# Performance work log

Hardware: AMD Instinct MI355X
Metric: run time of the kernel (lower is better)

The kernel has to match this reference:

```python
import jax, jax.numpy as jnp
import numpy as np
import math

B, N, HIDDEN = 2, 2048, 896
H_Q, H_KV, D = 14, 2, 64
ROPE_BASE = 1000000.0


def setup_inputs() -> dict:
    key = jax.random.key(0)
    ks = jax.random.split(key, 6)
    s = 0.02  # typical init scale for transformer weights
    return {
        "hidden_states": jax.random.normal(ks[0], (B, N, HIDDEN), jnp.float32),
        "position_ids": jnp.broadcast_to(jnp.arange(N, dtype=jnp.int32), (B, N)),
        "q_w": jax.random.normal(ks[1], (HIDDEN, H_Q * D), jnp.float32) * s,
        "q_b": jnp.zeros((H_Q * D,), jnp.float32),
        "k_w": jax.random.normal(ks[2], (HIDDEN, H_KV * D), jnp.float32) * s,
        "k_b": jnp.zeros((H_KV * D,), jnp.float32),
        "v_w": jax.random.normal(ks[3], (HIDDEN, H_KV * D), jnp.float32) * s,
        "v_b": jnp.zeros((H_KV * D,), jnp.float32),
        "o_w": jax.random.normal(ks[4], (H_Q * D, HIDDEN), jnp.float32) * s,
    }


def _rope(x, cos, sin):
    # rotate_half: [x1, x2] -> [-x2, x1]
    x1, x2 = jnp.split(x, 2, axis=-1)
    return x * cos + jnp.concatenate([-x2, x1], axis=-1) * sin


def reference(hidden_states, position_ids, q_w, q_b, k_w, k_b, v_w, v_b, o_w):
    Bs, Ns, _ = hidden_states.shape
    g = H_Q // H_KV  # heads per KV group (GQA)
    # QKV projections -> [B, H, N, d]
    Q = (hidden_states @ q_w + q_b).reshape(Bs, Ns, H_Q, D).transpose(0, 2, 1, 3)
    K = (hidden_states @ k_w + k_b).reshape(Bs, Ns, H_KV, D).transpose(0, 2, 1, 3)
    V = (hidden_states @ v_w + v_b).reshape(Bs, Ns, H_KV, D).transpose(0, 2, 1, 3)
    # RoPE (NTK base=1e6), cached cos/sin gathered by position_ids
    inv_freq = 1.0 / (ROPE_BASE ** (jnp.arange(0, D, 2, dtype=jnp.float32) / D))
    freqs = position_ids.astype(jnp.float32)[..., None] * inv_freq  # [B, N, D/2]
    emb = jnp.concatenate([freqs, freqs], axis=-1)  # [B, N, D]
    cos = jnp.cos(emb)[:, None]  # [B, 1, N, D]
    sin = jnp.sin(emb)[:, None]
    Q = _rope(Q, cos, sin)
    K = _rope(K, cos, sin)
    # GQA attention without materializing expanded K/V: group Q by KV head
    Qg = Q.reshape(Bs, H_KV, g, Ns, D)
    scale = 1.0 / math.sqrt(D)
    S = jnp.einsum('bkgqd,bknd->bkgqn', Qg, K) * scale  # [B, Hkv, g, Nq, Nk]
    # kv_cache=None => q_global_start = 0 => standard causal mask
    causal = jnp.arange(Ns)[:, None] >= jnp.arange(Ns)[None, :]
    S = jnp.where(causal[None, None, None], S, -jnp.inf)
    # stable softmax matching the module's online-softmax result (l + 1e-8)
    m = jnp.max(S, axis=-1, keepdims=True)
    e = jnp.exp(S - m)
    l = jnp.sum(e, axis=-1, keepdims=True)
    O = jnp.einsum('bkgqn,bknd->bkgqd', e, V) / (l + 1e-8)
    O = O.reshape(Bs, H_Q, Ns, D).transpose(0, 2, 1, 3).reshape(Bs, Ns, H_Q * D)
    return O @ o_w  # [B, N, hidden]
```

## Files before the change

kernel.cpp:

```cpp
#include <hip/hip_runtime.h>
#include <math.h>

#define BB 2
#define NN 2048
#define HID 896
#define HQ 14
#define HKV 2
#define DD 64
#define QKV_COLS 1152
#define QSCALE 0.18033688011112042f

typedef __bf16 bf16x8 __attribute__((ext_vector_type(8)));
typedef float f32x4 __attribute__((ext_vector_type(4)));

__device__ inline ushort f2bs(float f) {
  uint u = __builtin_bit_cast(uint, f);
  u += 0x7FFFu + ((u >> 16) & 1u);
  return (ushort)(u >> 16);
}
__device__ inline float bs2f(ushort u) {
  return __builtin_bit_cast(float, (uint)u << 16);
}

__device__ inline void gload16(const ushort* g, ushort* l) {
  __builtin_amdgcn_global_load_lds(
      (const __attribute__((address_space(1))) uint*)g,
      (__attribute__((address_space(3))) uint*)l, 16, 0, 0);
}

__device__ inline float dpp_fmax16(float x) {
  int v;
  v = __builtin_amdgcn_update_dpp(0, __builtin_bit_cast(int, x), 0xB1, 0xF, 0xF, true);
  x = fmaxf(x, __builtin_bit_cast(float, v));
  v = __builtin_amdgcn_update_dpp(0, __builtin_bit_cast(int, x), 0x4E, 0xF, 0xF, true);
  x = fmaxf(x, __builtin_bit_cast(float, v));
  v = __builtin_amdgcn_update_dpp(0, __builtin_bit_cast(int, x), 0x124, 0xF, 0xF, true);
  x = fmaxf(x, __builtin_bit_cast(float, v));
  v = __builtin_amdgcn_update_dpp(0, __builtin_bit_cast(int, x), 0x128, 0xF, 0xF, true);
  x = fmaxf(x, __builtin_bit_cast(float, v));
  return x;
}
__device__ inline float dpp_fadd16(float x) {
  int v;
  v = __builtin_amdgcn_update_dpp(0, __builtin_bit_cast(int, x), 0xB1, 0xF, 0xF, true);
  x += __builtin_bit_cast(float, v);
  v = __builtin_amdgcn_update_dpp(0, __builtin_bit_cast(int, x), 0x4E, 0xF, 0xF, true);
  x += __builtin_bit_cast(float, v);
  v = __builtin_amdgcn_update_dpp(0, __builtin_bit_cast(int, x), 0x124, 0xF, 0xF, true);
  x += __builtin_bit_cast(float, v);
  v = __builtin_amdgcn_update_dpp(0, __builtin_bit_cast(int, x), 0x128, 0xF, 0xF, true);
  x += __builtin_bit_cast(float, v);
  return x;
}

__global__ __launch_bounds__(256)
void prep_kernel(const float* __restrict__ hid, const int* __restrict__ pos,
                 const float* __restrict__ qw, const float* __restrict__ kw,
                 const float* __restrict__ vw, const float* __restrict__ ow,
                 const float* __restrict__ qb, const float* __restrict__ kb,
                 const float* __restrict__ vb,
                 ushort* __restrict__ Ah, ushort* __restrict__ WqkvT,
                 ushort* __restrict__ WoT, float2* __restrict__ tab,
                 float* __restrict__ biasQ)
{
  __shared__ float tile[32][33];
  const int blk = blockIdx.x, t = threadIdx.x;
  if (blk < 3584) {
    int i = blk * 256 + t;
    float4 v = ((const float4*)hid)[i];
    ushort4 o;
    o.x = f2bs(v.x); o.y = f2bs(v.y); o.z = f2bs(v.z); o.w = f2bs(v.w);
    ((ushort4*)Ah)[i] = o;
  } else if (blk < 5376) {
    const float* src; int N, n0, drow, k0;
    if (blk < 4592) {
      int idx = blk - 3584;
      int bx = idx % 36; k0 = (idx / 36) * 32;
      if (bx < 28)      { src = qw; N = 896; n0 = bx * 32;        drow = n0; }
      else if (bx < 32) { src = kw; N = 128; n0 = (bx - 28) * 32; drow = 896 + n0; }
      else              { src = vw; N = 128; n0 = (bx - 32) * 32; drow = 1024 + n0; }
    } else {
      int idx = blk - 4592;
      src = ow; N = 896; n0 = (idx % 28) * 32; k0 = (idx / 28) * 32; drow = n0;
    }
    ushort* dst = (blk < 4592) ? WqkvT : WoT;
    const int tx = t & 31, ty = t >> 5;
#pragma unroll
    for (int i = 0; i < 32; i += 8)
      tile[ty + i][tx] = src[(size_t)(k0 + ty + i) * N + n0 + tx];
    __syncthreads();
#pragma unroll
    for (int i = 0; i < 32; i += 8)
      dst[(size_t)(drow + ty + i) * HID + k0 + tx] = f2bs(tile[tx][ty + i]);
  } else if (blk < 5888) {
    int idx = (blk - 5376) * 256 + t;
    int m = idx >> 5, f = idx & 31;
    float inv = exp2f(-(float)f * (19.9315685693241741f / 32.0f));
    float ang = (float)pos[m] * inv;
    float sv, cv;
    sincosf(ang, &sv, &cv);
    tab[idx] = make_float2(cv, sv);
  } else {
    int i = (blk - 5888) * 256 + t;
    if (i < QKV_COLS)
      biasQ[i] = (i < 896) ? qb[i] : (i < 1024 ? kb[i - 896] : vb[i - 1024]);
  }
}

__global__ __launch_bounds__(256)
void gemm_qkv_rope(const ushort* __restrict__ A, const ushort* __restrict__ Bt,
                   const float* __restrict__ biasQ, const float2* __restrict__ tab,
                   ushort* __restrict__ Qo, ushort* __restrict__ Ko,
                   ushort* __restrict__ Vto)
{
  __shared__ ushort smem[9216];
  ushort* As = smem;
  ushort* Bs = smem + 2048;
  const int bx = blockIdx.x;
  const int n0 = bx * 128;
  const int m0 = blockIdx.y * 64;
  const int t = threadIdx.x;
  const int w = t >> 6, lane = t & 63;
  const int quad = lane >> 4, nn = lane & 15;
  const int wm = (w & 1) * 32, wn = (w >> 1) * 64;

  f32x4 acc[2][4];
#pragma unroll
  for (int i = 0; i < 2; i++)
#pragma unroll
    for (int j = 0; j < 4; j++) acc[i][j] = (f32x4){0.f, 0.f, 0.f, 0.f};

  for (int k0 = 0; k0 < HID; k0 += 32) {
    __syncthreads();
#pragma unroll
    for (int c = 0; c < 3; c++) {
      int ch = w * 3 + c;
      int rr = (lane >> 2), cl = lane & 3;
      if (ch < 4) {
        int r = ch * 16 + rr;
        int cg = cl ^ ((r >> 1) & 3);
        gload16(A + (size_t)(m0 + r) * HID + k0 + cg * 8, &As[r * 32 + cl * 8]);
      } else {
        int r = (ch - 4) * 16 + rr;
        int cg = cl ^ ((r >> 1) & 3);
        gload16(Bt + (size_t)(n0 + r) * HID + k0 + cg * 8, &Bs[r * 32 + cl * 8]);
      }
    }
    __syncthreads();

    bf16x8 aF[2], bF[4];
#pragma unroll
    for (int i = 0; i < 2; i++) {
      int ra = wm + i * 16 + nn;
      aF[i] = *(const bf16x8*)(&As[ra * 32 + (quad ^ ((ra >> 1) & 3)) * 8]);
    }
#pragma unroll
    for (int j = 0; j < 4; j++) {
      int rb = wn + j * 16 + nn;
      bF[j] = *(const bf16x8*)(&Bs[rb * 32 + (quad ^ ((rb >> 1) & 3)) * 8]);
    }
#pragma unroll
    for (int i = 0; i < 2; i++)
#pragma unroll
      for (int j = 0; j < 4; j++)
        acc[i][j] = __builtin_amdgcn_mfma_f32_16x16x32_bf16(aF[i], bF[j], acc[i][j], 0, 0, 0);
  }

  float bv[4];
#pragma unroll
  for (int j = 0; j < 4; j++) bv[j] = biasQ[n0 + wn + j * 16 + nn];

  if (bx < 8) {
    const float qs = (bx < 7) ? QSCALE : 1.0f;
    __syncthreads();
    const int ht = w >> 1;
    ushort* T = smem + ht * 4224;
#pragma unroll
    for (int i = 0; i < 2; i++) {
#pragma unroll
      for (int r = 0; r < 4; r++) {
        int row = wm + i * 16 + quad * 4 + r;
        int m = m0 + row;
        float2 cs0 = tab[m * 32 + nn];
        float2 cs1 = tab[m * 32 + 16 + nn];
        float x0 = (acc[i][0][r] + bv[0]) * qs;
        float x1 = (acc[i][1][r] + bv[1]) * qs;
        float x2 = (acc[i][2][r] + bv[2]) * qs;
        float x3 = (acc[i][3][r] + bv[3]) * qs;
        T[row * 66 + nn]      = f2bs(x0 * cs0.x - x2 * cs0.y);
        T[row * 66 + 16 + nn] = f2bs(x1 * cs1.x - x3 * cs1.y);
        T[row * 66 + 32 + nn] = f2bs(x2 * cs0.x + x0 * cs0.y);
        T[row * 66 + 48 + nn] = f2bs(x3 * cs1.x + x1 * cs1.y);
      }
    }
    __syncthreads();
    const int ht2 = t >> 7, tl = t & 127, row2 = tl >> 1, col0 = (tl & 1) * 32;
    const int m = m0 + row2, b = m >> 11, n = m & (NN - 1);
    const int hg = bx * 2 + ht2;
    ushort* dst = (hg < HQ)
        ? Qo + ((size_t)(b * HQ + hg) * NN + n) * DD + col0
        : Ko + ((size_t)(b * HKV + (hg - HQ)) * NN + n) * DD + col0;
    const ushort* src = smem + ht2 * 4224 + row2 * 66 + col0;
#pragma unroll
    for (int u = 0; u < 4; u++) ((uint4*)dst)[u] = ((const uint4*)src)[u];
  } else {
    __syncthreads();
    const int kvh = wn >> 6;
    ushort* T = smem + kvh * (64 * 72);
#pragma unroll
    for (int j = 0; j < 4; j++) {
      int dd = j * 16 + nn;
      float bvj = bv[j];
#pragma unroll
      for (int i = 0; i < 2; i++) {
        int mloc = wm + i * 16 + quad * 4;
        ushort4 pk;
        pk.x = f2bs(acc[i][j][0] + bvj);
        pk.y = f2bs(acc[i][j][1] + bvj);
        pk.z = f2bs(acc[i][j][2] + bvj);
        pk.w = f2bs(acc[i][j][3] + bvj);
        *(ushort4*)(&T[dd * 72 + mloc]) = pk;
      }
    }
    __syncthreads();
    const int head = t >> 7, dd2 = (t >> 1) & 63, seg = t & 1;
    const int b = m0 >> 11, nbase = (m0 & (NN - 1)) + seg * 32;
    const ushort* src = smem + head * (64 * 72) + dd2 * 72 + seg * 32;
    ushort* d = Vto + ((size_t)(b * HKV + head) * DD + dd2) * NN + nbase;
#pragma unroll
    for (int u = 0; u < 4; u++) ((uint4*)d)[u] = ((const uint4*)src)[u];
  }
}

__global__ __launch_bounds__(256)
void gemm_o(const ushort* __restrict__ A, const ushort* __restrict__ Bt,
            float* __restrict__ out)
{
  const int n0 = blockIdx.x * 128;
  const int m0 = blockIdx.y * 64;
  __shared__ ushort As[64 * 32];
  __shared__ ushort Bs[128 * 32];
  const int t = threadIdx.x;
  const int w = t >> 6, lane = t & 63;
  const int quad = lane >> 4, nn = lane & 15;
  const int wm = (w & 1) * 32, wn = (w >> 1) * 64;

  f32x4 acc[2][4];
#pragma unroll
  for (int i = 0; i < 2; i++)
#pragma unroll
    for (int j = 0; j < 4; j++) acc[i][j] = (f32x4){0.f, 0.f, 0.f, 0.f};

  for (int k0 = 0; k0 < HID; k0 += 32) {
    __syncthreads();
#pragma unroll
    for (int c = 0; c < 3; c++) {
      int ch = w * 3 + c;
      int rr = (lane >> 2), cl = lane & 3;
      if (ch < 4) {
        int r = ch * 16 + rr;
        int cg = cl ^ ((r >> 1) & 3);
        gload16(A + (size_t)(m0 + r) * HID + k0 + cg * 8, &As[r * 32 + cl * 8]);
      } else {
        int r = (ch - 4) * 16 + rr;
        int cg = cl ^ ((r >> 1) & 3);
        gload16(Bt + (size_t)(n0 + r) * HID + k0 + cg * 8, &Bs[r * 32 + cl * 8]);
      }
    }
    __syncthreads();

    bf16x8 aF[2], bF[4];
#pragma unroll
    for (int i = 0; i < 2; i++) {
      int ra = wm + i * 16 + nn;
      aF[i] = *(const bf16x8*)(&As[ra * 32 + (quad ^ ((ra >> 1) & 3)) * 8]);
    }
#pragma unroll
    for (int j = 0; j < 4; j++) {
      int rb = wn + j * 16 + nn;
      bF[j] = *(const bf16x8*)(&Bs[rb * 32 + (quad ^ ((rb >> 1) & 3)) * 8]);
    }
#pragma unroll
    for (int i = 0; i < 2; i++)
#pragma unroll
      for (int j = 0; j < 4; j++)
        acc[i][j] = __builtin_amdgcn_mfma_f32_16x16x32_bf16(aF[i], bF[j], acc[i][j], 0, 0, 0);
  }

#pragma unroll
  for (int j = 0; j < 4; j++) {
    const int col = n0 + wn + j * 16 + nn;
#pragma unroll
    for (int i = 0; i < 2; i++) {
      const int row = m0 + wm + i * 16 + quad * 4;
#pragma unroll
      for (int r = 0; r < 4; r++)
        out[(size_t)(row + r) * HID + col] = acc[i][j][r];
    }
  }
}

template <bool DIAG>
__device__ __forceinline__ void attn_step(
    int j, int qt, int quad, int nn,
    const ushort* __restrict__ Kb, const ushort* __restrict__ Vtb,
    ushort* __restrict__ Ps, const bf16x8 (&aQ)[2][2],
    f32x4 (&acc)[2][4], float (&mst)[2][4], float (&lac)[2][4])
{
  bf16x8 bk0[4], bk1[4];
#pragma unroll
  for (int ct = 0; ct < 4; ct++) {
    const ushort* kr = Kb + (size_t)(j * 64 + ct * 16 + nn) * DD;
    bk0[ct] = *(const bf16x8*)(kr + quad * 8);
    bk1[ct] = *(const bf16x8*)(kr + 32 + quad * 8);
  }
  bf16x8 bv0[4], bv1[4];
#pragma unroll
  for (int dt = 0; dt < 4; dt++) {
    const ushort* vr = Vtb + (size_t)(dt * 16 + nn) * NN + j * 64;
    bv0[dt] = *(const bf16x8*)(vr + quad * 8);
    bv1[dt] = *(const bf16x8*)(vr + 32 + quad * 8);
  }

  f32x4 s[2][4];
#pragma unroll
  for (int ct = 0; ct < 4; ct++)
#pragma unroll
    for (int mt = 0; mt < 2; mt++) {
      f32x4 cc = __builtin_amdgcn_mfma_f32_16x16x32_bf16(
          aQ[mt][0], bk0[ct], (f32x4){0.f, 0.f, 0.f, 0.f}, 0, 0, 0);
      s[mt][ct] = __builtin_amdgcn_mfma_f32_16x16x32_bf16(aQ[mt][1], bk1[ct], cc, 0, 0, 0);
    }

  if (DIAG) {
    const int keyb = j * 64 + nn;
    const int qb_ = qt * 32 + quad * 4;
#pragma unroll
    for (int mt = 0; mt < 2; mt++)
#pragma unroll
      for (int ct = 0; ct < 4; ct++)
#pragma unroll
        for (int r = 0; r < 4; r++)
          if (keyb + ct * 16 > qb_ + mt * 16 + r) s[mt][ct][r] = -1e30f;
  }

#pragma unroll
  for (int mt = 0; mt < 2; mt++)
#pragma unroll
    for (int r = 0; r < 4; r++) {
      float mx = fmaxf(fmaxf(s[mt][0][r], s[mt][1][r]), fmaxf(s[mt][2][r], s[mt][3][r]));
      mx = dpp_fmax16(mx);
      float mn = fmaxf(mst[mt][r], mx);
      float alpha = exp2f(mst[mt][r] - mn);
      mst[mt][r] = mn;
      float ll = 0.f;
#pragma unroll
      for (int ct = 0; ct < 4; ct++) {
        float p = exp2f(s[mt][ct][r] - mn);
        s[mt][ct][r] = p;
        ll += p;
      }
      lac[mt][r] = lac[mt][r] * alpha + ll;
#pragma unroll
      for (int dt = 0; dt < 4; dt++) acc[mt][dt][r] *= alpha;
    }

#pragma unroll
  for (int mt = 0; mt < 2; mt++)
#pragma unroll
    for (int ct = 0; ct < 4; ct++)
#pragma unroll
      for (int r = 0; r < 4; r++)
        Ps[(mt * 16 + quad * 4 + r) * 66 + ct * 16 + nn] = f2bs(s[mt][ct][r]);

#pragma unroll
  for (int mt = 0; mt < 2; mt++) {
    bf16x8 aP0 = *(const bf16x8*)(&Ps[(mt * 16 + nn) * 66 + quad * 8]);
    bf16x8 aP1 = *(const bf16x8*)(&Ps[(mt * 16 + nn) * 66 + 32 + quad * 8]);
#pragma unroll
    for (int dt = 0; dt < 4; dt++) {
      acc[mt][dt] = __builtin_amdgcn_mfma_f32_16x16x32_bf16(aP0, bv0[dt], acc[mt][dt], 0, 0, 0);
      acc[mt][dt] = __builtin_amdgcn_mfma_f32_16x16x32_bf16(aP1, bv1[dt], acc[mt][dt], 0, 0, 0);
    }
  }
}

__global__ __launch_bounds__(64, 3)
void attn_kernel(const ushort* __restrict__ Q, const ushort* __restrict__ K,
                 const ushort* __restrict__ Vt, ushort* __restrict__ O,
                 ushort* __restrict__ Opart, float* __restrict__ mpart,
                 float* __restrict__ lpart)
{
  const int u = 107 - (int)blockIdx.x;
  int qt, c;
  if (u < 28)      { qt = u; c = 0; }
  else if (u < 84) { int v = u - 28; qt = 28 + (v >> 1); c = v & 1; }
  else             { int v = u - 84; qt = 56 + v / 3; c = v - (v / 3) * 3; }
  const int h = blockIdx.y, b = blockIdx.z;
  const int kvh = h / (HQ / HKV);
  const int q0 = qt * 32;
  const int jmax = qt >> 1;
  const int nc = jmax / 14 + 1;
  const int jlo = c * 14;
  const int jhi = min(jmax, jlo + 13);
  const bool hasdiag = (jhi == jmax);
  const int jB = hasdiag ? jmax : jhi + 1;

  __shared__ ushort Ps[32 * 66];

  const int lane = threadIdx.x;
  const int quad = lane >> 4, nn = lane & 15;

  const ushort* Qb = Q + ((size_t)(b * HQ + h) * NN + q0) * DD;
  bf16x8 aQ[2][2];
#pragma unroll
  for (int mt = 0; mt < 2; mt++)
#pragma unroll
    for (int ks = 0; ks < 2; ks++)
      aQ[mt][ks] = *(const bf16x8*)(Qb + (size_t)(mt * 16 + nn) * DD + ks * 32 + quad * 8);

  const ushort* Kb  = K  + (size_t)(b * HKV + kvh) * NN * DD;
  const ushort* Vtb = Vt + (size_t)(b * HKV + kvh) * DD * NN;

  f32x4 acc[2][4];
#pragma unroll
  for (int mt = 0; mt < 2; mt++)
#pragma unroll
    for (int dt = 0; dt < 4; dt++) acc[mt][dt] = (f32x4){0.f, 0.f, 0.f, 0.f};
  float mst[2][4], lac[2][4];
#pragma unroll
  for (int mt = 0; mt < 2; mt++)
#pragma unroll
    for (int r = 0; r < 4; r++) { mst[mt][r] = -1e30f; lac[mt][r] = 0.f; }

  for (int j = jlo; j < jB; j++)
    attn_step<false>(j, qt, quad, nn, Kb, Vtb, Ps, aQ, acc, mst, lac);
  if (hasdiag)
    attn_step<true>(jmax, qt, quad, nn, Kb, Vtb, Ps, aQ, acc, mst, lac);

  float ltot[2][4];
#pragma unroll
  for (int mt = 0; mt < 2; mt++)
#pragma unroll
    for (int r = 0; r < 4; r++) ltot[mt][r] = dpp_fadd16(lac[mt][r]);

  if (nc == 1) {
#pragma unroll
    for (int mt = 0; mt < 2; mt++)
#pragma unroll
      for (int r = 0; r < 4; r++) {
        float linv = 1.f / (ltot[mt][r] + 1e-8f);
#pragma unroll
        for (int dt = 0; dt < 4; dt++)
          O[(size_t)(b * NN + q0 + mt * 16 + quad * 4 + r) * HID + h * DD + dt * 16 + nn] =
              f2bs(acc[mt][dt][r] * linv);
      }
  } else {
    const int off = (qt < 56) ? (qt - 28) * 2 : 56 + (qt - 56) * 3;
    const int p = (b * HQ + h) * 80 + off + c;
    ushort* Op = Opart + (size_t)p * 2048;
#pragma unroll
    for (int mt = 0; mt < 2; mt++)
#pragma unroll
      for (int r = 0; r < 4; r++) {
#pragma unroll
        for (int dt = 0; dt < 4; dt++)
          Op[(mt * 16 + quad * 4 + r) * 64 + dt * 16 + nn] = f2bs(acc[mt][dt][r]);
        if (nn == 0) {
          mpart[(size_t)p * 32 + mt * 16 + quad * 4 + r] = mst[mt][r];
          lpart[(size_t)p * 32 + mt * 16 + quad * 4 + r] = ltot[mt][r];
        }
      }
  }
}

__global__ __launch_bounds__(256)
void attn_reduce_kernel(const ushort* __restrict__ Opart, const float* __restrict__ mpart,
                        const float* __restrict__ lpart, ushort* __restrict__ O)
{
  const int qt = 28 + blockIdx.x;
  const int h = blockIdx.y, b = blockIdx.z;
  const int nc = (qt < 56) ? 2 : 3;
  const int off = (qt < 56) ? (qt - 28) * 2 : 56 + (qt - 56) * 3;
  const int pb = (b * HQ + h) * 80 + off;
  const int t = threadIdx.x;
  const int row = t >> 3, seg = t & 7;

  float mv[3], lv[3];
  float M = -1e30f;
  for (int c = 0; c < nc; c++) {
    mv[c] = mpart[(size_t)(pb + c) * 32 + row];
    lv[c] = lpart[(size_t)(pb + c) * 32 + row];
    M = fmaxf(M, mv[c]);
  }
  float l = 0.f, wv[3];
  for (int c = 0; c < nc; c++) { wv[c] = exp2f(mv[c] - M); l += lv[c] * wv[c]; }
  const float linv = 1.f / (l + 1e-8f);

  float av[8];
#pragma unroll
  for (int k = 0; k < 8; k++) av[k] = 0.f;
  for (int c = 0; c < nc; c++) {
    const ushort* Op = Opart + (size_t)(pb + c) * 2048 + row * 64 + seg * 8;
#pragma unroll
    for (int k = 0; k < 8; k++) av[k] += wv[c] * bs2f(Op[k]);
  }
  ushort ov[8];
#pragma unroll
  for (int k = 0; k < 8; k++) ov[k] = f2bs(av[k] * linv);
  ushort* Od = O + (size_t)(b * NN + qt * 32 + row) * HID + h * DD + seg * 8;
  *(uint4*)Od = *(uint4*)ov;
}

extern "C" void kernel_launch(void* const* d_in, const int* in_sizes, int n_in,
                              void* d_out, int out_size, void* d_ws, size_t ws_size,
                              hipStream_t stream)
{
  const float* hid = (const float*)d_in[0];
  const int*   pos = (const int*)  d_in[1];
  const float* qw  = (const float*)d_in[2];
  const float* qb  = (const float*)d_in[3];
  const float* kw  = (const float*)d_in[4];
  const float* kb  = (const float*)d_in[5];
  const float* vw  = (const float*)d_in[6];
  const float* vb  = (const float*)d_in[7];
  const float* ow  = (const float*)d_in[8];
  float* outp = (float*)d_out;

  ushort* WoT   = (ushort*)d_ws;
  ushort* WqkvT = WoT   + (size_t)HID * HID;
  ushort* Ah    = WqkvT + (size_t)QKV_COLS * HID;
  ushort* Qb    = Ah    + (size_t)4096 * HID;
  ushort* Kb    = Qb    + (size_t)BB * HQ  * NN * DD;
  ushort* Vtb   = Kb    + (size_t)BB * HKV * NN * DD;
  ushort* Ob    = Vtb   + (size_t)BB * HKV * NN * DD;
  float2* tab   = (float2*)(Ob + (size_t)4096 * HID);
  float*  biasQ = (float*)(tab + (size_t)4096 * 32);
  float*  mpart = biasQ + QKV_COLS;
  float*  lpart = mpart + (size_t)2240 * 32;
  ushort* Opart = WqkvT;

  prep_kernel<<<dim3(5893), 256, 0, stream>>>(hid, pos, qw, kw, vw, ow, qb, kb, vb,
                                              Ah, WqkvT, WoT, tab, biasQ);
  gemm_qkv_rope<<<dim3(9, 64), 256, 0, stream>>>(Ah, WqkvT, biasQ, tab, Qb, Kb, Vtb);
  attn_kernel<<<dim3(108, HQ, BB), 64, 0, stream>>>(Qb, Kb, Vtb, Ob, Opart, mpart, lpart);
  attn_reduce_kernel<<<dim3(36, HQ, BB), 256, 0, stream>>>(Opart, mpart, lpart, Ob);
  gemm_o<<<dim3(HID / 128, 64), 256, 0, stream>>>(Ob, WoT, outp);
}
```

Measured before the change: 215.7 us.

## Shrink attention query tile to 16 rows, add lazy rescale and MFMA priority

The attention kernel now processes 16 query rows per wave instead of 32. This doubles the grid to 216 blocks per head and raises the occupancy hint to 5 waves, with the split-K partition and reduce kernel remapped to match. It also skips the online-softmax rescale unless some row's max grows by more than 8, and raises wave priority around the MFMA sections. The cost is that each K/V tile loaded from global memory is reused across half as many queries, which doubles K/V traffic.

New measurement: 326.6 us. 51.4% more time.

```diff
diff --git a/kernel.cpp b/kernel.cpp
--- a/kernel.cpp
+++ b/kernel.cpp
@@ -301,11 +301,11 @@
 }
 
 template <bool DIAG>
-__device__ __forceinline__ void attn_step(
-    int j, int qt, int quad, int nn,
+__device__ __forceinline__ void attn_step16(
+    int j, int qglob, int quad, int nn,
     const ushort* __restrict__ Kb, const ushort* __restrict__ Vtb,
-    ushort* __restrict__ Ps, const bf16x8 (&aQ)[2][2],
-    f32x4 (&acc)[2][4], float (&mst)[2][4], float (&lac)[2][4])
+    ushort* __restrict__ Ps, const bf16x8 (&aQ)[2],
+    f32x4 (&acc)[4], float (&mst)[4], float (&lac)[4])
 {
   bf16x8 bk0[4], bk1[4];
 #pragma unroll
@@ -322,175 +322,169 @@
     bv1[dt] = *(const bf16x8*)(vr + 32 + quad * 8);
   }
 
-  f32x4 s[2][4];
-#pragma unroll
-  for (int ct = 0; ct < 4; ct++)
-#pragma unroll
-    for (int mt = 0; mt < 2; mt++) {
-      f32x4 cc = __builtin_amdgcn_mfma_f32_16x16x32_bf16(
-          aQ[mt][0], bk0[ct], (f32x4){0.f, 0.f, 0.f, 0.f}, 0, 0, 0);
-      s[mt][ct] = __builtin_amdgcn_mfma_f32_16x16x32_bf16(aQ[mt][1], bk1[ct], cc, 0, 0, 0);
-    }
+  f32x4 s[4];
+  __builtin_amdgcn_s_setprio(1);
+#pragma unroll
+  for (int ct = 0; ct < 4; ct++) {
+    f32x4 cc = __builtin_amdgcn_mfma_f32_16x16x32_bf16(
+        aQ[0], bk0[ct], (f32x4){0.f, 0.f, 0.f, 0.f}, 0, 0, 0);
+    s[ct] = __builtin_amdgcn_mfma_f32_16x16x32_bf16(aQ[1], bk1[ct], cc, 0, 0, 0);
+  }
+  __builtin_amdgcn_s_setprio(0);
 
   if (DIAG) {
     const int keyb = j * 64 + nn;
-    const int qb_ = qt * 32 + quad * 4;
-#pragma unroll
-    for (int mt = 0; mt < 2; mt++)
-#pragma unroll
-      for (int ct = 0; ct < 4; ct++)
-#pragma unroll
-        for (int r = 0; r < 4; r++)
-          if (keyb + ct * 16 > qb_ + mt * 16 + r) s[mt][ct][r] = -1e30f;
-  }
-
-#pragma unroll
-  for (int mt = 0; mt < 2; mt++)
+#pragma unroll
+    for (int ct = 0; ct < 4; ct++)
+#pragma unroll
+      for (int r = 0; r < 4; r++)
+        if (keyb + ct * 16 > qglob + r) s[ct][r] = -1e30f;
+  }
+
+  float mx[4];
+#pragma unroll
+  for (int r = 0; r < 4; r++)
+    mx[r] = dpp_fmax16(fmaxf(fmaxf(fmaxf(s[0][r], s[1][r]), s[2][r]), s[3][r]));
+
+  bool grow = false;
+#pragma unroll
+  for (int r = 0; r < 4; r++) grow = grow || (mx[r] > mst[r] + 8.0f);
+  if (__any(grow)) {
 #pragma unroll
     for (int r = 0; r < 4; r++) {
-      float mx = fmaxf(fmaxf(s[mt][0][r], s[mt][1][r]), fmaxf(s[mt][2][r], s[mt][3][r]));
-      mx = dpp_fmax16(mx);
-      float mn = fmaxf(mst[mt][r], mx);
-      float alpha = exp2f(mst[mt][r] - mn);
-      mst[mt][r] = mn;
-      float ll = 0.f;
-#pragma unroll
-      for (int ct = 0; ct < 4; ct++) {
-        float p = exp2f(s[mt][ct][r] - mn);
-        s[mt][ct][r] = p;
-        ll += p;
-      }
-      lac[mt][r] = lac[mt][r] * alpha + ll;
-#pragma unroll
-      for (int dt = 0; dt < 4; dt++) acc[mt][dt][r] *= alpha;
-    }
-
-#pragma unroll
-  for (int mt = 0; mt < 2; mt++)
-#pragma unroll
-    for (int ct = 0; ct < 4; ct++)
-#pragma unroll
-      for (int r = 0; r < 4; r++)
-        Ps[(mt * 16 + quad * 4 + r) * 66 + ct * 16 + nn] = f2bs(s[mt][ct][r]);
-
-#pragma unroll
-  for (int mt = 0; mt < 2; mt++) {
-    bf16x8 aP0 = *(const bf16x8*)(&Ps[(mt * 16 + nn) * 66 + quad * 8]);
-    bf16x8 aP1 = *(const bf16x8*)(&Ps[(mt * 16 + nn) * 66 + 32 + quad * 8]);
-#pragma unroll
-    for (int dt = 0; dt < 4; dt++) {
-      acc[mt][dt] = __builtin_amdgcn_mfma_f32_16x16x32_bf16(aP0, bv0[dt], acc[mt][dt], 0, 0, 0);
-      acc[mt][dt] = __builtin_amdgcn_mfma_f32_16x16x32_bf16(aP1, bv1[dt], acc[mt][dt], 0, 0, 0);
-    }
-  }
-}
-
-__global__ __launch_bounds__(64, 3)
+      float mn = fmaxf(mst[r], mx[r]);
+      float alpha = exp2f(mst[r] - mn);
+      mst[r] = mn;
+      lac[r] *= alpha;
+#pragma unroll
+      for (int dt = 0; dt < 4; dt++) acc[dt][r] *= alpha;
+    }
+  }
+
+#pragma unroll
+  for (int r = 0; r < 4; r++) {
+    float ll = 0.f;
+#pragma unroll
+    for (int ct = 0; ct < 4; ct++) {
+      float p = exp2f(s[ct][r] - mst[r]);
+      s[ct][r] = p;
+      ll += p;
+    }
+    lac[r] += ll;
+  }
+
+#pragma unroll
+  for (int ct = 0; ct < 4; ct++)
+#pragma unroll
+    for (int r = 0; r < 4; r++)
+      Ps[(quad * 4 + r) * 66 + ct * 16 + nn] = f2bs(s[ct][r]);
+
+  bf16x8 aP0 = *(const bf16x8*)(&Ps[nn * 66 + quad * 8]);
+  bf16x8 aP1 = *(const bf16x8*)(&Ps[nn * 66 + 32 + quad * 8]);
+  __builtin_amdgcn_s_setprio(1);
+#pragma unroll
+  for (int dt = 0; dt < 4; dt++) {
+    acc[dt] = __builtin_amdgcn_mfma_f32_16x16x32_bf16(aP0, bv0[dt], acc[dt], 0, 0, 0);
+    acc[dt] = __builtin_amdgcn_mfma_f32_16x16x32_bf16(aP1, bv1[dt], acc[dt], 0, 0, 0);
+  }
+  __builtin_amdgcn_s_setprio(0);
+}
+
+__global__ __launch_bounds__(64, 5)
 void attn_kernel(const ushort* __restrict__ Q, const ushort* __restrict__ K,
                  const ushort* __restrict__ Vt, ushort* __restrict__ O,
                  ushort* __restrict__ Opart, float* __restrict__ mpart,
                  float* __restrict__ lpart)
 {
-  const int u = 107 - (int)blockIdx.x;
+  const int u = 215 - (int)blockIdx.x;
   int qt, c;
-  if (u < 28)      { qt = u; c = 0; }
-  else if (u < 84) { int v = u - 28; qt = 28 + (v >> 1); c = v & 1; }
-  else             { int v = u - 84; qt = 56 + v / 3; c = v - (v / 3) * 3; }
+  if (u < 56)       { qt = u; c = 0; }
+  else if (u < 168) { int v = u - 56; qt = 56 + (v >> 1); c = v & 1; }
+  else              { int v = u - 168; qt = 112 + v / 3; c = v - (v / 3) * 3; }
   const int h = blockIdx.y, b = blockIdx.z;
   const int kvh = h / (HQ / HKV);
-  const int q0 = qt * 32;
-  const int jmax = qt >> 1;
+  const int q0 = qt * 16;
+  const int jmax = qt >> 2;
   const int nc = jmax / 14 + 1;
   const int jlo = c * 14;
   const int jhi = min(jmax, jlo + 13);
   const bool hasdiag = (jhi == jmax);
   const int jB = hasdiag ? jmax : jhi + 1;
 
-  __shared__ ushort Ps[32 * 66];
+  __shared__ ushort Ps[16 * 66];
 
   const int lane = threadIdx.x;
   const int quad = lane >> 4, nn = lane & 15;
+  const int qglob = q0 + quad * 4;
 
   const ushort* Qb = Q + ((size_t)(b * HQ + h) * NN + q0) * DD;
-  bf16x8 aQ[2][2];
-#pragma unroll
-  for (int mt = 0; mt < 2; mt++)
-#pragma unroll
-    for (int ks = 0; ks < 2; ks++)
-      aQ[mt][ks] = *(const bf16x8*)(Qb + (size_t)(mt * 16 + nn) * DD + ks * 32 + quad * 8);
+  bf16x8 aQ[2];
+#pragma unroll
+  for (int ks = 0; ks < 2; ks++)
+    aQ[ks] = *(const bf16x8*)(Qb + (size_t)nn * DD + ks * 32 + quad * 8);
 
   const ushort* Kb  = K  + (size_t)(b * HKV + kvh) * NN * DD;
   const ushort* Vtb = Vt + (size_t)(b * HKV + kvh) * DD * NN;
 
-  f32x4 acc[2][4];
-#pragma unroll
-  for (int mt = 0; mt < 2; mt++)
-#pragma unroll
-    for (int dt = 0; dt < 4; dt++) acc[mt][dt] = (f32x4){0.f, 0.f, 0.f, 0.f};
-  float mst[2][4], lac[2][4];
-#pragma unroll
-  for (int mt = 0; mt < 2; mt++)
-#pragma unroll
-    for (int r = 0; r < 4; r++) { mst[mt][r] = -1e30f; lac[mt][r] = 0.f; }
+  f32x4 acc[4];
+#pragma unroll
+  for (int dt = 0; dt < 4; dt++) acc[dt] = (f32x4){0.f, 0.f, 0.f, 0.f};
+  float mst[4], lac[4];
+#pragma unroll
+  for (int r = 0; r < 4; r++) { mst[r] = -1e30f; lac[r] = 0.f; }
 
   for (int j = jlo; j < jB; j++)
-    attn_step<false>(j, qt, quad, nn, Kb, Vtb, Ps, aQ, acc, mst, lac);
+    attn_step16<false>(j, qglob, quad, nn, Kb, Vtb, Ps, aQ, acc, mst, lac);
   if (hasdiag)
-    attn_step<true>(jmax, qt, quad, nn, Kb, Vtb, Ps, aQ, acc, mst, lac);
-
-  float ltot[2][4];
-#pragma unroll
-  for (int mt = 0; mt < 2; mt++)
-#pragma unroll
-    for (int r = 0; r < 4; r++) ltot[mt][r] = dpp_fadd16(lac[mt][r]);
+    attn_step16<true>(jmax, qglob, quad, nn, Kb, Vtb, Ps, aQ, acc, mst, lac);
+
+  float ltot[4];
+#pragma unroll
+  for (int r = 0; r < 4; r++) ltot[r] = dpp_fadd16(lac[r]);
 
   if (nc == 1) {
 #pragma unroll
-    for (int mt = 0; mt < 2; mt++)
-#pragma unroll
-      for (int r = 0; r < 4; r++) {
-        float linv = 1.f / (ltot[mt][r] + 1e-8f);
-#pragma unroll
-        for (int dt = 0; dt < 4; dt++)
-          O[(size_t)(b * NN + q0 + mt * 16 + quad * 4 + r) * HID + h * DD + dt * 16 + nn] =
-              f2bs(acc[mt][dt][r] * linv);
+    for (int r = 0; r < 4; r++) {
+      float linv = 1.f / (ltot[r] + 1e-8f);
+#pragma unroll
+      for (int dt = 0; dt < 4; dt++)
+        O[(size_t)(b * NN + q0 + quad * 4 + r) * HID + h * DD + dt * 16 + nn] =
+            f2bs(acc[dt][r] * linv);
+    }
+  } else {
+    const int off = (qt < 112) ? (qt - 56) * 2 : 112 + (qt - 112) * 3;
+    const int p = (b * HQ + h) * 160 + off + c;
+    ushort* Op = Opart + (size_t)p * 1024;
+#pragma unroll
+    for (int r = 0; r < 4; r++) {
+#pragma unroll
+      for (int dt = 0; dt < 4; dt++)
+        Op[(quad * 4 + r) * 64 + dt * 16 + nn] = f2bs(acc[dt][r]);
+      if (nn == 0) {
+        mpart[(size_t)p * 16 + quad * 4 + r] = mst[r];
+        lpart[(size_t)p * 16 + quad * 4 + r] = ltot[r];
       }
-  } else {
-    const int off = (qt < 56) ? (qt - 28) * 2 : 56 + (qt - 56) * 3;
-    const int p = (b * HQ + h) * 80 + off + c;
-    ushort* Op = Opart + (size_t)p * 2048;
-#pragma unroll
-    for (int mt = 0; mt < 2; mt++)
-#pragma unroll
-      for (int r = 0; r < 4; r++) {
-#pragma unroll
-        for (int dt = 0; dt < 4; dt++)
-          Op[(mt * 16 + quad * 4 + r) * 64 + dt * 16 + nn] = f2bs(acc[mt][dt][r]);
-        if (nn == 0) {
-          mpart[(size_t)p * 32 + mt * 16 + quad * 4 + r] = mst[mt][r];
-          lpart[(size_t)p * 32 + mt * 16 + quad * 4 + r] = ltot[mt][r];
-        }
-      }
-  }
-}
-
-__global__ __launch_bounds__(256)
+    }
+  }
+}
+
+__global__ __launch_bounds__(128)
 void attn_reduce_kernel(const ushort* __restrict__ Opart, const float* __restrict__ mpart,
                         const float* __restrict__ lpart, ushort* __restrict__ O)
 {
-  const int qt = 28 + blockIdx.x;
+  const int qt = 56 + blockIdx.x;
   const int h = blockIdx.y, b = blockIdx.z;
-  const int nc = (qt < 56) ? 2 : 3;
-  const int off = (qt < 56) ? (qt - 28) * 2 : 56 + (qt - 56) * 3;
-  const int pb = (b * HQ + h) * 80 + off;
+  const int nc = (qt < 112) ? 2 : 3;
+  const int off = (qt < 112) ? (qt - 56) * 2 : 112 + (qt - 112) * 3;
+  const int pb = (b * HQ + h) * 160 + off;
   const int t = threadIdx.x;
   const int row = t >> 3, seg = t & 7;
 
   float mv[3], lv[3];
   float M = -1e30f;
   for (int c = 0; c < nc; c++) {
-    mv[c] = mpart[(size_t)(pb + c) * 32 + row];
-    lv[c] = lpart[(size_t)(pb + c) * 32 + row];
+    mv[c] = mpart[(size_t)(pb + c) * 16 + row];
+    lv[c] = lpart[(size_t)(pb + c) * 16 + row];
     M = fmaxf(M, mv[c]);
   }
   float l = 0.f, wv[3];
@@ -501,14 +495,14 @@
 #pragma unroll
   for (int k = 0; k < 8; k++) av[k] = 0.f;
   for (int c = 0; c < nc; c++) {
-    const ushort* Op = Opart + (size_t)(pb + c) * 2048 + row * 64 + seg * 8;
+    const ushort* Op = Opart + (size_t)(pb + c) * 1024 + row * 64 + seg * 8;
 #pragma unroll
     for (int k = 0; k < 8; k++) av[k] += wv[c] * bs2f(Op[k]);
   }
   ushort ov[8];
 #pragma unroll
   for (int k = 0; k < 8; k++) ov[k] = f2bs(av[k] * linv);
-  ushort* Od = O + (size_t)(b * NN + qt * 32 + row) * HID + h * DD + seg * 8;
+  ushort* Od = O + (size_t)(b * NN + qt * 16 + row) * HID + h * DD + seg * 8;
   *(uint4*)Od = *(uint4*)ov;
 }
 
@@ -537,13 +531,13 @@
   float2* tab   = (float2*)(Ob + (size_t)4096 * HID);
   float*  biasQ = (float*)(tab + (size_t)4096 * 32);
   float*  mpart = biasQ + QKV_COLS;
-  float*  lpart = mpart + (size_t)2240 * 32;
+  float*  lpart = mpart + (size_t)4480 * 16;
   ushort* Opart = WqkvT;
 
   prep_kernel<<<dim3(5893), 256, 0, stream>>>(hid, pos, qw, kw, vw, ow, qb, kb, vb,
                                               Ah, WqkvT, WoT, tab, biasQ);
   gemm_qkv_rope<<<dim3(9, 64), 256, 0, stream>>>(Ah, WqkvT, biasQ, tab, Qb, Kb, Vtb);
-  attn_kernel<<<dim3(108, HQ, BB), 64, 0, stream>>>(Qb, Kb, Vtb, Ob, Opart, mpart, lpart);
-  attn_reduce_kernel<<<dim3(36, HQ, BB), 256, 0, stream>>>(Opart, mpart, lpart, Ob);
+  attn_kernel<<<dim3(216, HQ, BB), 64, 0, stream>>>(Qb, Kb, Vtb, Ob, Opart, mpart, lpart);
+  attn_reduce_kernel<<<dim3(72, HQ, BB), 128, 0, stream>>>(Opart, mpart, lpart, Ob);
   gemm_o<<<dim3(HID / 128, 64), 256, 0, stream>>>(Ob, WoT, outp);
 }
```

## Prefetch next K tile in registers, lazy softmax rescale, MFMA priority hints

Applied to the files above, without the earlier changes.

Loads the next iteration's K fragments during the current attention step, so global-load latency overlaps with compute. Online-softmax rescaling of the accumulators is skipped unless some row max grows by more than 8 in log2 units; the stale max is used otherwise. s_setprio is raised around the MFMA blocks. The prefetch raises register pressure and issues one extra K load at the end of each block. The lazy rescale relies on the bounded growth of exponent values staying within fp32 range.

Result: slower. 264.4 us (+22.6%).

```diff
diff --git a/kernel.cpp b/kernel.cpp
--- a/kernel.cpp
+++ b/kernel.cpp
@@ -302,18 +302,12 @@
 
 template <bool DIAG>
 __device__ __forceinline__ void attn_step(
-    int j, int qt, int quad, int nn,
+    int j, int jn, int qt, int quad, int nn,
     const ushort* __restrict__ Kb, const ushort* __restrict__ Vtb,
     ushort* __restrict__ Ps, const bf16x8 (&aQ)[2][2],
+    bf16x8 (&bk0)[4], bf16x8 (&bk1)[4],
     f32x4 (&acc)[2][4], float (&mst)[2][4], float (&lac)[2][4])
 {
-  bf16x8 bk0[4], bk1[4];
-#pragma unroll
-  for (int ct = 0; ct < 4; ct++) {
-    const ushort* kr = Kb + (size_t)(j * 64 + ct * 16 + nn) * DD;
-    bk0[ct] = *(const bf16x8*)(kr + quad * 8);
-    bk1[ct] = *(const bf16x8*)(kr + 32 + quad * 8);
-  }
   bf16x8 bv0[4], bv1[4];
 #pragma unroll
   for (int dt = 0; dt < 4; dt++) {
@@ -321,8 +315,16 @@
     bv0[dt] = *(const bf16x8*)(vr + quad * 8);
     bv1[dt] = *(const bf16x8*)(vr + 32 + quad * 8);
   }
+  bf16x8 nk0[4], nk1[4];
+#pragma unroll
+  for (int ct = 0; ct < 4; ct++) {
+    const ushort* kr = Kb + (size_t)(jn * 64 + ct * 16 + nn) * DD;
+    nk0[ct] = *(const bf16x8*)(kr + quad * 8);
+    nk1[ct] = *(const bf16x8*)(kr + 32 + quad * 8);
+  }
 
   f32x4 s[2][4];
+  __builtin_amdgcn_s_setprio(1);
 #pragma unroll
   for (int ct = 0; ct < 4; ct++)
 #pragma unroll
@@ -331,6 +333,7 @@
           aQ[mt][0], bk0[ct], (f32x4){0.f, 0.f, 0.f, 0.f}, 0, 0, 0);
       s[mt][ct] = __builtin_amdgcn_mfma_f32_16x16x32_bf16(aQ[mt][1], bk1[ct], cc, 0, 0, 0);
     }
+  __builtin_amdgcn_s_setprio(0);
 
   if (DIAG) {
     const int keyb = j * 64 + nn;
@@ -344,25 +347,45 @@
           if (keyb + ct * 16 > qb_ + mt * 16 + r) s[mt][ct][r] = -1e30f;
   }
 
+  float mx[2][4];
+#pragma unroll
+  for (int mt = 0; mt < 2; mt++)
+#pragma unroll
+    for (int r = 0; r < 4; r++)
+      mx[mt][r] = dpp_fmax16(
+          fmaxf(fmaxf(s[mt][0][r], s[mt][1][r]), fmaxf(s[mt][2][r], s[mt][3][r])));
+
+  bool grow = false;
+#pragma unroll
+  for (int mt = 0; mt < 2; mt++)
+#pragma unroll
+    for (int r = 0; r < 4; r++) grow = grow || (mx[mt][r] > mst[mt][r] + 8.0f);
+  if (__any(grow)) {
+#pragma unroll
+    for (int mt = 0; mt < 2; mt++)
+#pragma unroll
+      for (int r = 0; r < 4; r++) {
+        float mn = fmaxf(mst[mt][r], mx[mt][r]);
+        float alpha = exp2f(mst[mt][r] - mn);
+        mst[mt][r] = mn;
+        lac[mt][r] *= alpha;
+#pragma unroll
+        for (int dt = 0; dt < 4; dt++) acc[mt][dt][r] *= alpha;
+      }
+  }
+
 #pragma unroll
   for (int mt = 0; mt < 2; mt++)
 #pragma unroll
     for (int r = 0; r < 4; r++) {
-      float mx = fmaxf(fmaxf(s[mt][0][r], s[mt][1][r]), fmaxf(s[mt][2][r], s[mt][3][r]));
-      mx = dpp_fmax16(mx);
-      float mn = fmaxf(mst[mt][r], mx);
-      float alpha = exp2f(mst[mt][r] - mn);
-      mst[mt][r] = mn;
       float ll = 0.f;
 #pragma unroll
       for (int ct = 0; ct < 4; ct++) {
-        float p = exp2f(s[mt][ct][r] - mn);
+        float p = exp2f(s[mt][ct][r] - mst[mt][r]);
         s[mt][ct][r] = p;
         ll += p;
       }
-      lac[mt][r] = lac[mt][r] * alpha + ll;
-#pragma unroll
-      for (int dt = 0; dt < 4; dt++) acc[mt][dt][r] *= alpha;
+      lac[mt][r] += ll;
     }
 
 #pragma unroll
@@ -377,12 +400,17 @@
   for (int mt = 0; mt < 2; mt++) {
     bf16x8 aP0 = *(const bf16x8*)(&Ps[(mt * 16 + nn) * 66 + quad * 8]);
     bf16x8 aP1 = *(const bf16x8*)(&Ps[(mt * 16 + nn) * 66 + 32 + quad * 8]);
+    __builtin_amdgcn_s_setprio(1);
 #pragma unroll
     for (int dt = 0; dt < 4; dt++) {
       acc[mt][dt] = __builtin_amdgcn_mfma_f32_16x16x32_bf16(aP0, bv0[dt], acc[mt][dt], 0, 0, 0);
       acc[mt][dt] = __builtin_amdgcn_mfma_f32_16x16x32_bf16(aP1, bv1[dt], acc[mt][dt], 0, 0, 0);
     }
-  }
+    __builtin_amdgcn_s_setprio(0);
+  }
+
+#pragma unroll
+  for (int ct = 0; ct < 4; ct++) { bk0[ct] = nk0[ct]; bk1[ct] = nk1[ct]; }
 }
 
 __global__ __launch_bounds__(64, 3)
@@ -433,10 +461,18 @@
 #pragma unroll
     for (int r = 0; r < 4; r++) { mst[mt][r] = -1e30f; lac[mt][r] = 0.f; }
 
+  bf16x8 bk0[4], bk1[4];
+#pragma unroll
+  for (int ct = 0; ct < 4; ct++) {
+    const ushort* kr = Kb + (size_t)(jlo * 64 + ct * 16 + nn) * DD;
+    bk0[ct] = *(const bf16x8*)(kr + quad * 8);
+    bk1[ct] = *(const bf16x8*)(kr + 32 + quad * 8);
+  }
+
   for (int j = jlo; j < jB; j++)
-    attn_step<false>(j, qt, quad, nn, Kb, Vtb, Ps, aQ, acc, mst, lac);
+    attn_step<false>(j, j + 1, qt, quad, nn, Kb, Vtb, Ps, aQ, bk0, bk1, acc, mst, lac);
   if (hasdiag)
-    attn_step<true>(jmax, qt, quad, nn, Kb, Vtb, Ps, aQ, acc, mst, lac);
+    attn_step<true>(jmax, jmax, qt, quad, nn, Kb, Vtb, Ps, aQ, bk0, bk1, acc, mst, lac);
 
   float ltot[2][4];
 #pragma unroll
```

## Rewrite attention inner loop with transposed 32x32 MFMA and register-resident P

Applied to the files above, without the earlier changes.

The attention step now computes S^T = K·Q^T with 32x32x16 bf16 MFMAs, so each lane owns one query column. That turns the row max and row sum into in-register reductions plus one cross-half shuffle instead of DPP chains. P is converted to bf16 with packed converts and rearranged with permlane32 swaps to feed the PV MFMA directly, removing the LDS round trip through the Ps buffer. It also adds a lazy rescale that only updates the running max when it grows by more than 8 (log2 units), and sets wave priority around the MFMA blocks. The lazy rescale carries some accuracy risk if scores drift, and the 32x32 layout raises register pressure.

Measured after the change: 226.4 us. +4.9%, slower.

```diff
diff --git a/kernel.cpp b/kernel.cpp
--- a/kernel.cpp
+++ b/kernel.cpp
@@ -12,6 +12,8 @@
 
 typedef __bf16 bf16x8 __attribute__((ext_vector_type(8)));
 typedef float f32x4 __attribute__((ext_vector_type(4)));
+typedef float f32x16 __attribute__((ext_vector_type(16)));
+typedef uint u32x4 __attribute__((ext_vector_type(4)));
 
 __device__ inline ushort f2bs(float f) {
   uint u = __builtin_bit_cast(uint, f);
@@ -28,29 +30,13 @@
       (__attribute__((address_space(3))) uint*)l, 16, 0, 0);
 }
 
-__device__ inline float dpp_fmax16(float x) {
-  int v;
-  v = __builtin_amdgcn_update_dpp(0, __builtin_bit_cast(int, x), 0xB1, 0xF, 0xF, true);
-  x = fmaxf(x, __builtin_bit_cast(float, v));
-  v = __builtin_amdgcn_update_dpp(0, __builtin_bit_cast(int, x), 0x4E, 0xF, 0xF, true);
-  x = fmaxf(x, __builtin_bit_cast(float, v));
-  v = __builtin_amdgcn_update_dpp(0, __builtin_bit_cast(int, x), 0x124, 0xF, 0xF, true);
-  x = fmaxf(x, __builtin_bit_cast(float, v));
-  v = __builtin_amdgcn_update_dpp(0, __builtin_bit_cast(int, x), 0x128, 0xF, 0xF, true);
-  x = fmaxf(x, __builtin_bit_cast(float, v));
-  return x;
-}
-__device__ inline float dpp_fadd16(float x) {
-  int v;
-  v = __builtin_amdgcn_update_dpp(0, __builtin_bit_cast(int, x), 0xB1, 0xF, 0xF, true);
-  x += __builtin_bit_cast(float, v);
-  v = __builtin_amdgcn_update_dpp(0, __builtin_bit_cast(int, x), 0x4E, 0xF, 0xF, true);
-  x += __builtin_bit_cast(float, v);
-  v = __builtin_amdgcn_update_dpp(0, __builtin_bit_cast(int, x), 0x124, 0xF, 0xF, true);
-  x += __builtin_bit_cast(float, v);
-  v = __builtin_amdgcn_update_dpp(0, __builtin_bit_cast(int, x), 0x128, 0xF, 0xF, true);
-  x += __builtin_bit_cast(float, v);
-  return x;
+__device__ inline uint cvtpk(float lo, float hi) {
+  uint d;
+  asm("v_cvt_pk_bf16_f32 %0, %1, %2" : "=v"(d) : "v"(lo), "v"(hi));
+  return d;
+}
+__device__ inline void perm32swap(uint& a, uint& b) {
+  asm("v_permlane32_swap_b32 %0, %1" : "+v"(a), "+v"(b));
 }
 
 __global__ __launch_bounds__(256)
@@ -301,88 +287,110 @@
 }
 
 template <bool DIAG>
-__device__ __forceinline__ void attn_step(
-    int j, int qt, int quad, int nn,
+__device__ __forceinline__ void attn_step32(
+    int j, int qglob, int lo, int hi,
     const ushort* __restrict__ Kb, const ushort* __restrict__ Vtb,
-    ushort* __restrict__ Ps, const bf16x8 (&aQ)[2][2],
-    f32x4 (&acc)[2][4], float (&mst)[2][4], float (&lac)[2][4])
-{
-  bf16x8 bk0[4], bk1[4];
-#pragma unroll
-  for (int ct = 0; ct < 4; ct++) {
-    const ushort* kr = Kb + (size_t)(j * 64 + ct * 16 + nn) * DD;
-    bk0[ct] = *(const bf16x8*)(kr + quad * 8);
-    bk1[ct] = *(const bf16x8*)(kr + 32 + quad * 8);
-  }
-  bf16x8 bv0[4], bv1[4];
-#pragma unroll
-  for (int dt = 0; dt < 4; dt++) {
-    const ushort* vr = Vtb + (size_t)(dt * 16 + nn) * NN + j * 64;
-    bv0[dt] = *(const bf16x8*)(vr + quad * 8);
-    bv1[dt] = *(const bf16x8*)(vr + 32 + quad * 8);
-  }
-
-  f32x4 s[2][4];
-#pragma unroll
-  for (int ct = 0; ct < 4; ct++)
-#pragma unroll
-    for (int mt = 0; mt < 2; mt++) {
-      f32x4 cc = __builtin_amdgcn_mfma_f32_16x16x32_bf16(
-          aQ[mt][0], bk0[ct], (f32x4){0.f, 0.f, 0.f, 0.f}, 0, 0, 0);
-      s[mt][ct] = __builtin_amdgcn_mfma_f32_16x16x32_bf16(aQ[mt][1], bk1[ct], cc, 0, 0, 0);
-    }
+    const bf16x8 (&bQ)[4],
+    f32x16 (&accO)[2], float& mst, float& lac)
+{
+  bf16x8 aV[2][2][2];
+#pragma unroll
+  for (int dtile = 0; dtile < 2; dtile++)
+#pragma unroll
+    for (int t = 0; t < 2; t++)
+#pragma unroll
+      for (int ks = 0; ks < 2; ks++)
+        aV[dtile][t][ks] = *(const bf16x8*)(
+            Vtb + (size_t)(dtile * 32 + lo) * NN + j * 64 + t * 32 + ks * 16 + hi * 8);
+  bf16x8 aK[2][4];
+#pragma unroll
+  for (int t = 0; t < 2; t++)
+#pragma unroll
+    for (int s = 0; s < 4; s++)
+      aK[t][s] = *(const bf16x8*)(
+          Kb + (size_t)(j * 64 + t * 32 + lo) * DD + s * 16 + hi * 8);
+
+  f32x16 st[2];
+  __builtin_amdgcn_s_setprio(1);
+#pragma unroll
+  for (int t = 0; t < 2; t++) {
+    f32x16 z;
+#pragma unroll
+    for (int e = 0; e < 16; e++) z[e] = 0.f;
+#pragma unroll
+    for (int s = 0; s < 4; s++)
+      z = __builtin_amdgcn_mfma_f32_32x32x16_bf16(aK[t][s], bQ[s], z, 0, 0, 0);
+    st[t] = z;
+  }
+  __builtin_amdgcn_s_setprio(0);
 
   if (DIAG) {
-    const int keyb = j * 64 + nn;
-    const int qb_ = qt * 32 + quad * 4;
-#pragma unroll
-    for (int mt = 0; mt < 2; mt++)
-#pragma unroll
-      for (int ct = 0; ct < 4; ct++)
-#pragma unroll
-        for (int r = 0; r < 4; r++)
-          if (keyb + ct * 16 > qb_ + mt * 16 + r) s[mt][ct][r] = -1e30f;
-  }
-
-#pragma unroll
-  for (int mt = 0; mt < 2; mt++)
-#pragma unroll
-    for (int r = 0; r < 4; r++) {
-      float mx = fmaxf(fmaxf(s[mt][0][r], s[mt][1][r]), fmaxf(s[mt][2][r], s[mt][3][r]));
-      mx = dpp_fmax16(mx);
-      float mn = fmaxf(mst[mt][r], mx);
-      float alpha = exp2f(mst[mt][r] - mn);
-      mst[mt][r] = mn;
-      float ll = 0.f;
-#pragma unroll
-      for (int ct = 0; ct < 4; ct++) {
-        float p = exp2f(s[mt][ct][r] - mn);
-        s[mt][ct][r] = p;
-        ll += p;
-      }
-      lac[mt][r] = lac[mt][r] * alpha + ll;
-#pragma unroll
-      for (int dt = 0; dt < 4; dt++) acc[mt][dt][r] *= alpha;
-    }
-
-#pragma unroll
-  for (int mt = 0; mt < 2; mt++)
-#pragma unroll
-    for (int ct = 0; ct < 4; ct++)
-#pragma unroll
-      for (int r = 0; r < 4; r++)
-        Ps[(mt * 16 + quad * 4 + r) * 66 + ct * 16 + nn] = f2bs(s[mt][ct][r]);
-
-#pragma unroll
-  for (int mt = 0; mt < 2; mt++) {
-    bf16x8 aP0 = *(const bf16x8*)(&Ps[(mt * 16 + nn) * 66 + quad * 8]);
-    bf16x8 aP1 = *(const bf16x8*)(&Ps[(mt * 16 + nn) * 66 + 32 + quad * 8]);
-#pragma unroll
-    for (int dt = 0; dt < 4; dt++) {
-      acc[mt][dt] = __builtin_amdgcn_mfma_f32_16x16x32_bf16(aP0, bv0[dt], acc[mt][dt], 0, 0, 0);
-      acc[mt][dt] = __builtin_amdgcn_mfma_f32_16x16x32_bf16(aP1, bv1[dt], acc[mt][dt], 0, 0, 0);
-    }
-  }
+#pragma unroll
+    for (int t = 0; t < 2; t++)
+#pragma unroll
+      for (int e = 0; e < 16; e++) {
+        int key = j * 64 + t * 32 + (e & 3) + 8 * (e >> 2) + 4 * hi;
+        if (key > qglob) st[t][e] = -1e30f;
+      }
+  }
+
+  float red[16];
+#pragma unroll
+  for (int e = 0; e < 16; e++) red[e] = fmaxf(st[0][e], st[1][e]);
+#pragma unroll
+  for (int off = 8; off > 0; off >>= 1)
+#pragma unroll
+    for (int i = 0; i < off; i++) red[i] = fmaxf(red[i], red[i + off]);
+  float mx = fmaxf(red[0], __shfl_xor(red[0], 32));
+
+  if (__any(mx > mst + 8.0f)) {
+    float mn = fmaxf(mst, mx);
+    float alpha = exp2f(mst - mn);
+    mst = mn;
+    lac *= alpha;
+    accO[0] *= alpha;
+    accO[1] *= alpha;
+  }
+
+  f32x16 p[2];
+  float sred[16];
+#pragma unroll
+  for (int e = 0; e < 16; e++) {
+    p[0][e] = exp2f(st[0][e] - mst);
+    p[1][e] = exp2f(st[1][e] - mst);
+    sred[e] = p[0][e] + p[1][e];
+  }
+#pragma unroll
+  for (int off = 8; off > 0; off >>= 1)
+#pragma unroll
+    for (int i = 0; i < off; i++) sred[i] += sred[i + off];
+  lac += sred[0];
+
+  bf16x8 pf[2][2];
+#pragma unroll
+  for (int t = 0; t < 2; t++)
+#pragma unroll
+    for (int w = 0; w < 2; w++) {
+      int e0 = w * 8;
+      uint c01 = cvtpk(p[t][e0 + 0], p[t][e0 + 1]);
+      uint c23 = cvtpk(p[t][e0 + 2], p[t][e0 + 3]);
+      uint c45 = cvtpk(p[t][e0 + 4], p[t][e0 + 5]);
+      uint c67 = cvtpk(p[t][e0 + 6], p[t][e0 + 7]);
+      perm32swap(c01, c45);
+      perm32swap(c23, c67);
+      pf[t][w] = __builtin_bit_cast(bf16x8, (u32x4){c01, c23, c45, c67});
+    }
+
+  __builtin_amdgcn_s_setprio(1);
+#pragma unroll
+  for (int dtile = 0; dtile < 2; dtile++)
+#pragma unroll
+    for (int t = 0; t < 2; t++)
+#pragma unroll
+      for (int w = 0; w < 2; w++)
+        accO[dtile] = __builtin_amdgcn_mfma_f32_32x32x16_bf16(
+            aV[dtile][t][w], pf[t][w], accO[dtile], 0, 0, 0);
+  __builtin_amdgcn_s_setprio(0);
 }
 
 __global__ __launch_bounds__(64, 3)
@@ -406,71 +414,66 @@
   const bool hasdiag = (jhi == jmax);
   const int jB = hasdiag ? jmax : jhi + 1;
 
-  __shared__ ushort Ps[32 * 66];
-
   const int lane = threadIdx.x;
-  const int quad = lane >> 4, nn = lane & 15;
+  const int lo = lane & 31, hi = lane >> 5;
+  const int qglob = q0 + lo;
 
   const ushort* Qb = Q + ((size_t)(b * HQ + h) * NN + q0) * DD;
-  bf16x8 aQ[2][2];
-#pragma unroll
-  for (int mt = 0; mt < 2; mt++)
-#pragma unroll
-    for (int ks = 0; ks < 2; ks++)
-      aQ[mt][ks] = *(const bf16x8*)(Qb + (size_t)(mt * 16 + nn) * DD + ks * 32 + quad * 8);
+  bf16x8 bQ[4];
+#pragma unroll
+  for (int s = 0; s < 4; s++)
+    bQ[s] = *(const bf16x8*)(Qb + (size_t)lo * DD + s * 16 + hi * 8);
 
   const ushort* Kb  = K  + (size_t)(b * HKV + kvh) * NN * DD;
   const ushort* Vtb = Vt + (size_t)(b * HKV + kvh) * DD * NN;
 
-  f32x4 acc[2][4];
-#pragma unroll
-  for (int mt = 0; mt < 2; mt++)
-#pragma unroll
-    for (int dt = 0; dt < 4; dt++) acc[mt][dt] = (f32x4){0.f, 0.f, 0.f, 0.f};
-  float mst[2][4], lac[2][4];
-#pragma unroll
-  for (int mt = 0; mt < 2; mt++)
-#pragma unroll
-    for (int r = 0; r < 4; r++) { mst[mt][r] = -1e30f; lac[mt][r] = 0.f; }
+  f32x16 accO[2];
+#pragma unroll
+  for (int dtile = 0; dtile < 2; dtile++)
+#pragma unroll
+    for (int e = 0; e < 16; e++) accO[dtile][e] = 0.f;
+  float mst = -1e30f, lac = 0.f;
 
   for (int j = jlo; j < jB; j++)
-    attn_step<false>(j, qt, quad, nn, Kb, Vtb, Ps, aQ, acc, mst, lac);
+    attn_step32<false>(j, qglob, lo, hi, Kb, Vtb, bQ, accO, mst, lac);
   if (hasdiag)
-    attn_step<true>(jmax, qt, quad, nn, Kb, Vtb, Ps, aQ, acc, mst, lac);
-
-  float ltot[2][4];
-#pragma unroll
-  for (int mt = 0; mt < 2; mt++)
-#pragma unroll
-    for (int r = 0; r < 4; r++) ltot[mt][r] = dpp_fadd16(lac[mt][r]);
+    attn_step32<true>(jmax, qglob, lo, hi, Kb, Vtb, bQ, accO, mst, lac);
+
+  const float ltot = lac + __shfl_xor(lac, 32);
 
   if (nc == 1) {
-#pragma unroll
-    for (int mt = 0; mt < 2; mt++)
-#pragma unroll
-      for (int r = 0; r < 4; r++) {
-        float linv = 1.f / (ltot[mt][r] + 1e-8f);
-#pragma unroll
-        for (int dt = 0; dt < 4; dt++)
-          O[(size_t)(b * NN + q0 + mt * 16 + quad * 4 + r) * HID + h * DD + dt * 16 + nn] =
-              f2bs(acc[mt][dt][r] * linv);
+    const float linv = 1.f / (ltot + 1e-8f);
+    ushort* Orow = O + (size_t)(b * NN + q0 + lo) * HID + h * DD;
+#pragma unroll
+    for (int dtile = 0; dtile < 2; dtile++)
+#pragma unroll
+      for (int g = 0; g < 4; g++) {
+        ushort4 ov;
+        ov.x = f2bs(accO[dtile][g * 4 + 0] * linv);
+        ov.y = f2bs(accO[dtile][g * 4 + 1] * linv);
+        ov.z = f2bs(accO[dtile][g * 4 + 2] * linv);
+        ov.w = f2bs(accO[dtile][g * 4 + 3] * linv);
+        *(ushort4*)(Orow + dtile * 32 + g * 8 + 4 * hi) = ov;
       }
   } else {
     const int off = (qt < 56) ? (qt - 28) * 2 : 56 + (qt - 56) * 3;
     const int p = (b * HQ + h) * 80 + off + c;
-    ushort* Op = Opart + (size_t)p * 2048;
-#pragma unroll
-    for (int mt = 0; mt < 2; mt++)
-#pragma unroll
-      for (int r = 0; r < 4; r++) {
-#pragma unroll
-        for (int dt = 0; dt < 4; dt++)
-          Op[(mt * 16 + quad * 4 + r) * 64 + dt * 16 + nn] = f2bs(acc[mt][dt][r]);
-        if (nn == 0) {
-          mpart[(size_t)p * 32 + mt * 16 + quad * 4 + r] = mst[mt][r];
-          lpart[(size_t)p * 32 + mt * 16 + quad * 4 + r] = ltot[mt][r];
-        }
-      }
+    ushort* Op = Opart + (size_t)p * 2048 + lo * 64;
+#pragma unroll
+    for (int dtile = 0; dtile < 2; dtile++)
+#pragma unroll
+      for (int g = 0; g < 4; g++) {
+        ushort4 ov;
+        ov.x = f2bs(accO[dtile][g * 4 + 0]);
+        ov.y = f2bs(accO[dtile][g * 4 + 1]);
+        ov.z = f2bs(accO[dtile][g * 4 + 2]);
+        ov.w = f2bs(accO[dtile][g * 4 + 3]);
+        *(ushort4*)(Op + dtile * 32 + g * 8 + 4 * hi) = ov;
+      }
+    if (hi == 0) {
+      mpart[(size_t)p * 32 + lo] = mst;
+      lpart[(size_t)p * 32 + lo] = ltot;
+    }
   }
 }
 
```
